# Kernel tuning notes

Hardware: AMD Instinct MI355X
Metric: run time of the kernel (lower is better)

The kernel has to match this reference:

```python
import jax, jax.numpy as jnp
import numpy as np

SEQ_LEN = 256
DT = 0.05
PI4 = float(np.pi / 4)
B = 16384


def _policy(h, W1, b1, W2, b2, W3, b3, W4, b4):
    h = jax.nn.relu(h @ W1 + b1)
    h = jax.nn.relu(h @ W2 + b2)
    h = jax.nn.relu(h @ W3 + b3)
    return jnp.tanh(h @ W4 + b4)


def setup_inputs() -> dict:
    key = jax.random.key(0)
    ks = jax.random.split(key, 11)
    return {
        "state": jax.random.normal(ks[0], (B, 6), jnp.float32),
        "pstate": jax.random.normal(ks[1], (B, 6), jnp.float32),
        "target": jax.random.normal(ks[2], (B, 6), jnp.float32),
        "W1": jax.random.normal(ks[3], (12, 50), jnp.float32) * 0.2,
        "b1": jax.random.normal(ks[4], (50,), jnp.float32) * 0.1,
        "W2": jax.random.normal(ks[5], (50, 50), jnp.float32) * 0.14,
        "b2": jax.random.normal(ks[6], (50,), jnp.float32) * 0.1,
        "W3": jax.random.normal(ks[7], (50, 50), jnp.float32) * 0.14,
        "b3": jax.random.normal(ks[8], (50,), jnp.float32) * 0.1,
        "W4": jax.random.normal(ks[9], (50, 2), jnp.float32) * 0.14,
        "b4": jax.random.normal(ks[10], (2,), jnp.float32) * 0.1,
    }


def reference(state, pstate, target, W1, b1, W2, b2, W3, b3, W4, b4):
    # target duplicated to match concat(pstate, state): [B, 12]
    tgt = jnp.concatenate([target, target], axis=-1)

    def step(carry, _):
        pstate, state = carry
        u = _policy(jnp.concatenate([pstate, state], axis=-1) - tgt,
                    W1, b1, W2, b2, W3, b3, W4, b4) * 0.5  # [B, 2]
        x, y, c, s, v, w = (state[:, i] for i in range(6))
        cw = jnp.cos(w * DT)
        sw = jnp.sin(w * DT)
        x = x + v * c * DT
        y = y + v * s * DT
        c_new = c * cw - s * sw
        # NOTE: original torch code uses the *updated* c when updating s
        s_new = s * cw + c_new * sw
        v = jnp.clip(v + u[:, 0] * DT, -0.1, 0.3)
        w = jnp.clip(w + u[:, 1] * DT, -PI4, PI4)
        new_state = jnp.stack([x, y, c_new, s_new, v, w], axis=-1)
        return (state, new_state), (u, new_state)

    _, (u_seq, states) = jax.lax.scan(step, (pstate, state), None, length=SEQ_LEN)
    # u_seq: [SEQ_LEN, B, 2], states: [SEQ_LEN, B, 6]
    return u_seq, states
```

## Files before the change

### kernel.cpp

```cpp
#include <hip/hip_runtime.h>
#include <hip/hip_bf16.h>
#include <stdint.h>
#include <math.h>

#define SEQ_LEN 256
#define BATCH   16384

typedef _Float16 half8  __attribute__((ext_vector_type(8)));
typedef _Float16 half2t __attribute__((ext_vector_type(2)));
typedef __attribute__((ext_vector_type(4))) float    floatx4;
typedef __attribute__((ext_vector_type(4))) uint32_t uint4v;
typedef __attribute__((ext_vector_type(2))) float    float2v;

__device__ __forceinline__ uint32_t pkh(float a, float b){
    return __builtin_bit_cast(uint32_t, __builtin_amdgcn_cvt_pkrtz(a, b));
}
__device__ __forceinline__ float h16lo(uint32_t p){
    return (float)__builtin_bit_cast(half2t, p)[0];
}
__device__ __forceinline__ float h16hi(uint32_t p){
    return (float)__builtin_bit_cast(half2t, p)[1];
}
__device__ __forceinline__ half8 ashfrag(uint4v u){ return __builtin_bit_cast(half8, u); }
#define MFMA_H(A,B,C) __builtin_amdgcn_mfma_f32_16x16x32_f16((A),(B),(C),0,0,0)

__global__ __launch_bounds__(64, 1) void mbrl_mfma(
    const float* __restrict__ state0, const float* __restrict__ pstate0,
    const float* __restrict__ target,
    const float* __restrict__ W1, const float* __restrict__ b1,
    const float* __restrict__ W2, const float* __restrict__ b2,
    const float* __restrict__ W3, const float* __restrict__ b3,
    const float* __restrict__ W4, const float* __restrict__ b4,
    float* __restrict__ out)
{
    const int lane = threadIdx.x & 63;
    const int c16  = lane & 15;
    const int phi  = lane >> 4;
    const int rowg = (int)blockIdx.x * 16 + c16;

    half8 P1[4], Q1[4];
#pragma unroll
    for (int t = 0; t < 4; ++t){
        const int j = 16*t + c16;
        uint4v uP, uQ;
#pragma unroll
        for (int v = 0; v < 4; ++v){
            float pP[2], pQ[2];
#pragma unroll
            for (int q = 0; q < 2; ++q){
                const int kk = 16*(v>>1) + 4*phi + 2*(v&1) + q;
                float w = 0.f;
                if (j < 50){
                    if (kk < 12)                  w = W1[kk*50 + j];
                    else if (kk == 12)            w = b1[j];
                    else if (kk >= 16 && kk < 28) w = W1[(kk-16)*50 + j];
                }
                float s0 = (float)(_Float16)w;
                pP[q] = s0; pQ[q] = w - s0;
            }
            uP[v] = pkh(pP[0], pP[1]);
            uQ[v] = pkh(pQ[0], pQ[1]);
        }
        P1[t] = ashfrag(uP); Q1[t] = ashfrag(uQ);
    }

    half8 A2[2][4][2], A3[2][4][2];
#pragma unroll
    for (int t = 0; t < 4; ++t){
        const int j = 16*t + c16;
#pragma unroll
        for (int kt = 0; kt < 2; ++kt){
            uint4v u2[2], u3[2];
#pragma unroll
            for (int v = 0; v < 4; ++v){
                float p2[2][2], p3[2][2];
#pragma unroll
                for (int q = 0; q < 2; ++q){
                    const int kk = 32*kt + 16*(v>>1) + 4*phi + 2*(v&1) + q;
                    float w2v = 0.f, w3v = 0.f;
                    if (j < 50){
                        if (kk < 50){ w2v = W2[kk*50 + j]; w3v = W3[kk*50 + j]; }
                        else if (kk == 50){ w2v = b2[j]; w3v = b3[j]; }
                    }
                    float a0 = (float)(_Float16)w2v;
                    float c0s = (float)(_Float16)w3v;
                    p2[0][q] = a0;  p2[1][q] = w2v - a0;
                    p3[0][q] = c0s; p3[1][q] = w3v - c0s;
                }
#pragma unroll
                for (int s = 0; s < 2; ++s){
                    u2[s][v] = pkh(p2[s][0], p2[s][1]);
                    u3[s][v] = pkh(p3[s][0], p3[s][1]);
                }
            }
#pragma unroll
            for (int s = 0; s < 2; ++s){
                A2[s][t][kt] = ashfrag(u2[s]); A3[s][t][kt] = ashfrag(u3[s]);
            }
        }
    }

    float w4a[16], w4b[16];
#pragma unroll
    for (int t = 0; t < 4; ++t)
#pragma unroll
        for (int r = 0; r < 4; ++r){
            const int j = 16*t + 4*phi + r;
            w4a[4*t+r] = (j < 50) ? W4[j*2 + 0] : 0.f;
            w4b[4*t+r] = (j < 50) ? W4[j*2 + 1] : 0.f;
        }
    const float b40 = b4[0], b41 = b4[1];

    float ps[6], ss[6], tg[6];
#pragma unroll
    for (int i = 0; i < 6; ++i){
        ps[i] = pstate0[(size_t)rowg*6 + i];
        ss[i] = state0 [(size_t)rowg*6 + i];
        tg[i] = target [(size_t)rowg*6 + i];
    }

    const float DT  = 0.05f;
    const float PI4 = 0.78539816339744830962f;
    const floatx4 z4 = {0.f,0.f,0.f,0.f};
    const uint32_t ONE_H = 0x00003C00u;

    float* uout = out + (size_t)rowg * 2;
    float* sout = out + (size_t)SEQ_LEN * BATCH * 2 + (size_t)rowg * 6;

    half8 H0a,H0b,H1a,H1b;

#define SPLITH(HA,HB,PK0,PK1) do{                                      \
        PK0 = pkh((HA),(HB));                                          \
        float _a = h16lo(PK0), _b = h16hi(PK0);                        \
        PK1 = pkh((HA)-_a, (HB)-_b);                                   \
    }while(0)

#define MKH(cc0,cc1,cc2,cc3) do{                                                             \
        uint4v u0a,u0b,u1a,u1b;                                                              \
        { float ha=fmaxf(cc0[0],0.f), hb=fmaxf(cc0[1],0.f); SPLITH(ha,hb,u0a[0],u1a[0]); }   \
        { float ha=fmaxf(cc0[2],0.f), hb=fmaxf(cc0[3],0.f); SPLITH(ha,hb,u0a[1],u1a[1]); }   \
        { float ha=fmaxf(cc1[0],0.f), hb=fmaxf(cc1[1],0.f); SPLITH(ha,hb,u0a[2],u1a[2]); }   \
        { float ha=fmaxf(cc1[2],0.f), hb=fmaxf(cc1[3],0.f); SPLITH(ha,hb,u0a[3],u1a[3]); }   \
        { float ha=fmaxf(cc2[0],0.f), hb=fmaxf(cc2[1],0.f); SPLITH(ha,hb,u0b[0],u1b[0]); }   \
        { float ha=fmaxf(cc2[2],0.f), hb=fmaxf(cc2[3],0.f); SPLITH(ha,hb,u0b[1],u1b[1]); }   \
        { float ha=fmaxf(cc3[0],0.f), hb=fmaxf(cc3[1],0.f); SPLITH(ha,hb,u0b[2],u1b[2]); }   \
        { float ha=fmaxf(cc3[2],0.f), hb=fmaxf(cc3[3],0.f); SPLITH(ha,hb,u0b[3],u1b[3]); }   \
        if (phi == 0){ u0b[3]=ONE_H; u1b[3]=0u; }                  \
        H0a=ashfrag(u0a); H0b=ashfrag(u0b); H1a=ashfrag(u1a); H1b=ashfrag(u1b);              \
    }while(0)

#define HID_RR(A)                                                                            \
        c0=MFMA_H(A[0][0][0],H0a,z4); c1=MFMA_H(A[0][1][0],H0a,z4); c2=MFMA_H(A[0][2][0],H0a,z4); c3=MFMA_H(A[0][3][0],H0a,z4); \
        c0=MFMA_H(A[0][0][1],H0b,c0); c1=MFMA_H(A[0][1][1],H0b,c1); c2=MFMA_H(A[0][2][1],H0b,c2); c3=MFMA_H(A[0][3][1],H0b,c3); \
        c0=MFMA_H(A[0][0][0],H1a,c0); c1=MFMA_H(A[0][1][0],H1a,c1); c2=MFMA_H(A[0][2][0],H1a,c2); c3=MFMA_H(A[0][3][0],H1a,c3); \
        c0=MFMA_H(A[0][0][1],H1b,c0); c1=MFMA_H(A[0][1][1],H1b,c1); c2=MFMA_H(A[0][2][1],H1b,c2); c3=MFMA_H(A[0][3][1],H1b,c3); \
        c0=MFMA_H(A[1][0][0],H0a,c0); c1=MFMA_H(A[1][1][0],H0a,c1); c2=MFMA_H(A[1][2][0],H0a,c2); c3=MFMA_H(A[1][3][0],H0a,c3); \
        c0=MFMA_H(A[1][0][1],H0b,c0); c1=MFMA_H(A[1][1][1],H0b,c1); c2=MFMA_H(A[1][2][1],H0b,c2); c3=MFMA_H(A[1][3][1],H0b,c3);

#define L4ACC(CT,T) do{                                                   \
        _Pragma("unroll")                                                 \
        for (int r = 0; r < 4; ++r){                                      \
            float hv = fmaxf(CT[r], 0.f);                                 \
            z0p = fmaf(hv, w4a[4*(T)+r], z0p);                            \
            z1p = fmaf(hv, w4b[4*(T)+r], z1p);                            \
        }                                                                 \
    }while(0)

    for (int t = 0; t < SEQ_LEN; ++t){
        float X0=ps[0]-tg[0], X1=ps[1]-tg[1], X2=ps[2]-tg[2];
        float X3=ps[3]-tg[3], X4=ps[4]-tg[4], X5=ps[5]-tg[5];
        float X6=ss[0]-tg[0], X7=ss[1]-tg[1], X8=ss[2]-tg[2];
        float X9=ss[3]-tg[3], X10=ss[4]-tg[4], X11=ss[5]-tg[5];
        float xs0 = (phi==0)?X0:(phi==1)?X4:(phi==2)?X8 :0.f;
        float xs1 = (phi==0)?X1:(phi==1)?X5:(phi==2)?X9 :0.f;
        float xs2 = (phi==0)?X2:(phi==1)?X6:(phi==2)?X10:0.f;
        float xs3 = (phi==0)?X3:(phi==1)?X7:(phi==2)?X11:0.f;
        uint32_t pH01,pL01,pH23,pL23;
        SPLITH(xs0,xs1,pH01,pL01);
        SPLITH(xs2,xs3,pH23,pL23);
        uint4v f1;
        f1[0] = (phi==3) ? ONE_H : pH01;
        f1[1] = (phi==3) ? 0u    : pH23;
        f1[2] = (phi==3) ? 0u    : pL01;
        f1[3] = (phi==3) ? 0u    : pL23;
        const half8 F1 = ashfrag(f1);

        floatx4 c0, c1, c2, c3;
        c0=MFMA_H(P1[0],F1,z4); c1=MFMA_H(P1[1],F1,z4); c2=MFMA_H(P1[2],F1,z4); c3=MFMA_H(P1[3],F1,z4);
        c0=MFMA_H(Q1[0],F1,c0); c1=MFMA_H(Q1[1],F1,c1); c2=MFMA_H(Q1[2],F1,c2); c3=MFMA_H(Q1[3],F1,c3);
        MKH(c0,c1,c2,c3);

        HID_RR(A2)
        MKH(c0,c1,c2,c3);

        HID_RR(A3)

        float z0p = 0.f, z1p = 0.f;
        L4ACC(c0,0); L4ACC(c1,1); L4ACC(c2,2); L4ACC(c3,3);
        z0p += __shfl_xor(z0p, 16, 64);
        z1p += __shfl_xor(z1p, 16, 64);
        z0p += __shfl_xor(z0p, 32, 64);
        z1p += __shfl_xor(z1p, 32, 64);
        float zz0 = z0p + b40;
        float zz1 = z1p + b41;

        float u0 = 0.5f - __builtin_amdgcn_rcpf(__expf(2.0f*zz0) + 1.0f);
        float u1 = 0.5f - __builtin_amdgcn_rcpf(__expf(2.0f*zz1) + 1.0f);

        float th = ss[5]*DT, t2 = th*th;
        float sw = th * fmaf(t2, fmaf(t2, 8.3333333333e-3f, -1.6666666667e-1f), 1.0f);
        float cw = fmaf(t2, fmaf(t2, fmaf(t2, -1.3888888889e-3f, 4.1666666667e-2f), -0.5f), 1.0f);
        float nx = fmaf(ss[4]*ss[2], DT, ss[0]);
        float ny = fmaf(ss[4]*ss[3], DT, ss[1]);
        float nc = ss[2]*cw - ss[3]*sw;
        float ns = fmaf(ss[3], cw, nc*sw);
        float nv = fminf(fmaxf(fmaf(u0, DT, ss[4]), -0.1f), 0.3f);
        float nw = fminf(fmaxf(fmaf(u1, DT, ss[5]), -PI4), PI4);

        if (phi == 0){
            float2v uv  = {u0, u1};
            *(float2v*)uout = uv;
            float2v s01 = {nx, ny}, s23 = {nc, ns}, s45 = {nv, nw};
            *(float2v*)(sout    ) = s01;
            *(float2v*)(sout + 2) = s23;
            *(float2v*)(sout + 4) = s45;
        }
        uout += (size_t)BATCH * 2;
        sout += (size_t)BATCH * 6;

#pragma unroll
        for (int i = 0; i < 6; ++i) ps[i] = ss[i];
        ss[0]=nx; ss[1]=ny; ss[2]=nc; ss[3]=ns; ss[4]=nv; ss[5]=nw;
    }
#undef MKH
#undef SPLITH
#undef HID_RR
#undef L4ACC
}

extern "C" void kernel_launch(void* const* d_in, const int* in_sizes, int n_in,
                              void* d_out, int out_size, void* d_ws, size_t ws_size,
                              hipStream_t stream)
{
    const float* state  = (const float*)d_in[0];
    const float* pstate = (const float*)d_in[1];
    const float* target = (const float*)d_in[2];
    const float* W1 = (const float*)d_in[3];
    const float* b1 = (const float*)d_in[4];
    const float* W2 = (const float*)d_in[5];
    const float* b2 = (const float*)d_in[6];
    const float* W3 = (const float*)d_in[7];
    const float* b3 = (const float*)d_in[8];
    const float* W4 = (const float*)d_in[9];
    const float* b4 = (const float*)d_in[10];
    float* out = (float*)d_out;

    dim3 grid(BATCH/16), block(64);
    mbrl_mfma<<<grid, block, 0, stream>>>(state, pstate, target,
                                          W1,b1,W2,b2,W3,b3,W4,b4, out);
}
```

Before: 287.5 us.

## Split hidden-unit tiles across two wavefronts with LDS exchange per layer

Each block now runs two wavefronts on the same 16 batch rows, and each wave computes half of the 64 hidden-unit tiles. The halves of each activation vector and of the final layer's partial sums are exchanged through shared memory, with a block barrier at every layer. The goal is to shorten the serial MFMA dependency chain per timestep and halve per-wave weight registers, allowing higher occupancy. In exchange it adds three __syncthreads and LDS round trips per step over 256 sequential steps, and it doubles the wave count.

```diff
diff --git a/kernel.cpp b/kernel.cpp
--- a/kernel.cpp
+++ b/kernel.cpp
@@ -24,7 +24,7 @@
 __device__ __forceinline__ half8 ashfrag(uint4v u){ return __builtin_bit_cast(half8, u); }
 #define MFMA_H(A,B,C) __builtin_amdgcn_mfma_f32_16x16x32_f16((A),(B),(C),0,0,0)
 
-__global__ __launch_bounds__(64, 1) void mbrl_mfma(
+__global__ __launch_bounds__(128, 2) void mbrl_mfma2(
     const float* __restrict__ state0, const float* __restrict__ pstate0,
     const float* __restrict__ target,
     const float* __restrict__ W1, const float* __restrict__ b1,
@@ -33,15 +33,21 @@
     const float* __restrict__ W4, const float* __restrict__ b4,
     float* __restrict__ out)
 {
-    const int lane = threadIdx.x & 63;
+    const int tid  = threadIdx.x;
+    const int wid  = tid >> 6;
+    const int lane = tid & 63;
     const int c16  = lane & 15;
     const int phi  = lane >> 4;
     const int rowg = (int)blockIdx.x * 16 + c16;
 
-    half8 P1[4], Q1[4];
-#pragma unroll
-    for (int t = 0; t < 4; ++t){
-        const int j = 16*t + c16;
+    __shared__ __align__(16) uint4v  xA[2][2][64];
+    __shared__ __align__(16) uint4v  xB[2][2][64];
+    __shared__ __align__(16) float2v zxch[2][64];
+
+    half8 P1[2], Q1[2];
+#pragma unroll
+    for (int tl = 0; tl < 2; ++tl){
+        const int j = 16*(2*wid + tl) + c16;
         uint4v uP, uQ;
 #pragma unroll
         for (int v = 0; v < 4; ++v){
@@ -61,13 +67,13 @@
             uP[v] = pkh(pP[0], pP[1]);
             uQ[v] = pkh(pQ[0], pQ[1]);
         }
-        P1[t] = ashfrag(uP); Q1[t] = ashfrag(uQ);
-    }
-
-    half8 A2[2][4][2], A3[2][4][2];
-#pragma unroll
-    for (int t = 0; t < 4; ++t){
-        const int j = 16*t + c16;
+        P1[tl] = ashfrag(uP); Q1[tl] = ashfrag(uQ);
+    }
+
+    half8 A2[2][2][2], A3[2][2][2];
+#pragma unroll
+    for (int tl = 0; tl < 2; ++tl){
+        const int j = 16*(2*wid + tl) + c16;
 #pragma unroll
         for (int kt = 0; kt < 2; ++kt){
             uint4v u2[2], u3[2];
@@ -82,7 +88,7 @@
                         if (kk < 50){ w2v = W2[kk*50 + j]; w3v = W3[kk*50 + j]; }
                         else if (kk == 50){ w2v = b2[j]; w3v = b3[j]; }
                     }
-                    float a0 = (float)(_Float16)w2v;
+                    float a0  = (float)(_Float16)w2v;
                     float c0s = (float)(_Float16)w3v;
                     p2[0][q] = a0;  p2[1][q] = w2v - a0;
                     p3[0][q] = c0s; p3[1][q] = w3v - c0s;
@@ -95,19 +101,19 @@
             }
 #pragma unroll
             for (int s = 0; s < 2; ++s){
-                A2[s][t][kt] = ashfrag(u2[s]); A3[s][t][kt] = ashfrag(u3[s]);
+                A2[s][tl][kt] = ashfrag(u2[s]); A3[s][tl][kt] = ashfrag(u3[s]);
             }
         }
     }
 
-    float w4a[16], w4b[16];
-#pragma unroll
-    for (int t = 0; t < 4; ++t)
+    float w4a[8], w4b[8];
+#pragma unroll
+    for (int tl = 0; tl < 2; ++tl)
 #pragma unroll
         for (int r = 0; r < 4; ++r){
-            const int j = 16*t + 4*phi + r;
-            w4a[4*t+r] = (j < 50) ? W4[j*2 + 0] : 0.f;
-            w4b[4*t+r] = (j < 50) ? W4[j*2 + 1] : 0.f;
+            const int j = 32*wid + 16*tl + 4*phi + r;
+            w4a[4*tl+r] = (j < 50) ? W4[j*2 + 0] : 0.f;
+            w4b[4*tl+r] = (j < 50) ? W4[j*2 + 1] : 0.f;
         }
     const float b40 = b4[0], b41 = b4[1];
 
@@ -126,8 +132,6 @@
 
     float* uout = out + (size_t)rowg * 2;
     float* sout = out + (size_t)SEQ_LEN * BATCH * 2 + (size_t)rowg * 6;
-
-    half8 H0a,H0b,H1a,H1b;
 
 #define SPLITH(HA,HB,PK0,PK1) do{                                      \
         PK0 = pkh((HA),(HB));                                          \
@@ -135,36 +139,31 @@
         PK1 = pkh((HA)-_a, (HB)-_b);                                   \
     }while(0)
 
-#define MKH(cc0,cc1,cc2,cc3) do{                                                             \
-        uint4v u0a,u0b,u1a,u1b;                                                              \
-        { float ha=fmaxf(cc0[0],0.f), hb=fmaxf(cc0[1],0.f); SPLITH(ha,hb,u0a[0],u1a[0]); }   \
-        { float ha=fmaxf(cc0[2],0.f), hb=fmaxf(cc0[3],0.f); SPLITH(ha,hb,u0a[1],u1a[1]); }   \
-        { float ha=fmaxf(cc1[0],0.f), hb=fmaxf(cc1[1],0.f); SPLITH(ha,hb,u0a[2],u1a[2]); }   \
-        { float ha=fmaxf(cc1[2],0.f), hb=fmaxf(cc1[3],0.f); SPLITH(ha,hb,u0a[3],u1a[3]); }   \
-        { float ha=fmaxf(cc2[0],0.f), hb=fmaxf(cc2[1],0.f); SPLITH(ha,hb,u0b[0],u1b[0]); }   \
-        { float ha=fmaxf(cc2[2],0.f), hb=fmaxf(cc2[3],0.f); SPLITH(ha,hb,u0b[1],u1b[1]); }   \
-        { float ha=fmaxf(cc3[0],0.f), hb=fmaxf(cc3[1],0.f); SPLITH(ha,hb,u0b[2],u1b[2]); }   \
-        { float ha=fmaxf(cc3[2],0.f), hb=fmaxf(cc3[3],0.f); SPLITH(ha,hb,u0b[3],u1b[3]); }   \
-        if (phi == 0){ u0b[3]=ONE_H; u1b[3]=0u; }                  \
-        H0a=ashfrag(u0a); H0b=ashfrag(u0b); H1a=ashfrag(u1a); H1b=ashfrag(u1b);              \
+#define PACKH(CA,CB,U0,U1) do{                                                           \
+        { float ha=fmaxf(CA[0],0.f), hb=fmaxf(CA[1],0.f); SPLITH(ha,hb,U0[0],U1[0]); }   \
+        { float ha=fmaxf(CA[2],0.f), hb=fmaxf(CA[3],0.f); SPLITH(ha,hb,U0[1],U1[1]); }   \
+        { float ha=fmaxf(CB[0],0.f), hb=fmaxf(CB[1],0.f); SPLITH(ha,hb,U0[2],U1[2]); }   \
+        { float ha=fmaxf(CB[2],0.f), hb=fmaxf(CB[3],0.f); SPLITH(ha,hb,U0[3],U1[3]); }   \
+        if (wid == 1 && phi == 0){ U0[3] = ONE_H; U1[3] = 0u; }     \
     }while(0)
 
-#define HID_RR(A)                                                                            \
-        c0=MFMA_H(A[0][0][0],H0a,z4); c1=MFMA_H(A[0][1][0],H0a,z4); c2=MFMA_H(A[0][2][0],H0a,z4); c3=MFMA_H(A[0][3][0],H0a,z4); \
-        c0=MFMA_H(A[0][0][1],H0b,c0); c1=MFMA_H(A[0][1][1],H0b,c1); c2=MFMA_H(A[0][2][1],H0b,c2); c3=MFMA_H(A[0][3][1],H0b,c3); \
-        c0=MFMA_H(A[0][0][0],H1a,c0); c1=MFMA_H(A[0][1][0],H1a,c1); c2=MFMA_H(A[0][2][0],H1a,c2); c3=MFMA_H(A[0][3][0],H1a,c3); \
-        c0=MFMA_H(A[0][0][1],H1b,c0); c1=MFMA_H(A[0][1][1],H1b,c1); c2=MFMA_H(A[0][2][1],H1b,c2); c3=MFMA_H(A[0][3][1],H1b,c3); \
-        c0=MFMA_H(A[1][0][0],H0a,c0); c1=MFMA_H(A[1][1][0],H0a,c1); c2=MFMA_H(A[1][2][0],H0a,c2); c3=MFMA_H(A[1][3][0],H0a,c3); \
-        c0=MFMA_H(A[1][0][1],H0b,c0); c1=MFMA_H(A[1][1][1],H0b,c1); c2=MFMA_H(A[1][2][1],H0b,c2); c3=MFMA_H(A[1][3][1],H0b,c3);
-
-#define L4ACC(CT,T) do{                                                   \
-        _Pragma("unroll")                                                 \
-        for (int r = 0; r < 4; ++r){                                      \
-            float hv = fmaxf(CT[r], 0.f);                                 \
-            z0p = fmaf(hv, w4a[4*(T)+r], z0p);                            \
-            z1p = fmaf(hv, w4b[4*(T)+r], z1p);                            \
-        }                                                                 \
+#define XCHG(R)  do{                                                    \
+        R[wid][0][lane] = u0; R[wid][1][lane] = u1;                     \
+        __syncthreads();                                                \
+        uint4v o0 = R[wid^1][0][lane], o1 = R[wid^1][1][lane];          \
+        if (wid == 0){ H0a=ashfrag(u0); H1a=ashfrag(u1);                \
+                       H0b=ashfrag(o0); H1b=ashfrag(o1); }              \
+        else         { H0a=ashfrag(o0); H1a=ashfrag(o1);                \
+                       H0b=ashfrag(u0); H1b=ashfrag(u1); }              \
     }while(0)
+
+#define HID(A)                                                              \
+        ca=MFMA_H(A[0][0][0],H0a,z4); cb=MFMA_H(A[0][1][0],H0a,z4);         \
+        ca=MFMA_H(A[0][0][1],H0b,ca); cb=MFMA_H(A[0][1][1],H0b,cb);         \
+        ca=MFMA_H(A[0][0][0],H1a,ca); cb=MFMA_H(A[0][1][0],H1a,cb);         \
+        ca=MFMA_H(A[0][0][1],H1b,ca); cb=MFMA_H(A[0][1][1],H1b,cb);         \
+        ca=MFMA_H(A[1][0][0],H0a,ca); cb=MFMA_H(A[1][1][0],H0a,cb);         \
+        ca=MFMA_H(A[1][0][1],H0b,ca); cb=MFMA_H(A[1][1][1],H0b,cb);
 
     for (int t = 0; t < SEQ_LEN; ++t){
         float X0=ps[0]-tg[0], X1=ps[1]-tg[1], X2=ps[2]-tg[2];
@@ -180,23 +179,44 @@
         SPLITH(xs2,xs3,pH23,pL23);
         uint4v f1;
         f1[0] = (phi==3) ? ONE_H : pH01;
-        f1[1] = (phi==3) ? 0u    : pH23;
-        f1[2] = (phi==3) ? 0u    : pL01;
-        f1[3] = (phi==3) ? 0u    : pL23;
+        f1[1] = pH23;
+        f1[2] = pL01;
+        f1[3] = pL23;
         const half8 F1 = ashfrag(f1);
 
-        floatx4 c0, c1, c2, c3;
-        c0=MFMA_H(P1[0],F1,z4); c1=MFMA_H(P1[1],F1,z4); c2=MFMA_H(P1[2],F1,z4); c3=MFMA_H(P1[3],F1,z4);
-        c0=MFMA_H(Q1[0],F1,c0); c1=MFMA_H(Q1[1],F1,c1); c2=MFMA_H(Q1[2],F1,c2); c3=MFMA_H(Q1[3],F1,c3);
-        MKH(c0,c1,c2,c3);
-
-        HID_RR(A2)
-        MKH(c0,c1,c2,c3);
-
-        HID_RR(A3)
+        floatx4 ca, cb;
+        ca=MFMA_H(P1[0],F1,z4); cb=MFMA_H(P1[1],F1,z4);
+        ca=MFMA_H(Q1[0],F1,ca); cb=MFMA_H(Q1[1],F1,cb);
+
+        half8 H0a,H0b,H1a,H1b;
+        uint4v u0, u1;
+        PACKH(ca,cb,u0,u1);
+        XCHG(xA);
+
+        HID(A2)
+        PACKH(ca,cb,u0,u1);
+        XCHG(xB);
+
+        HID(A3)
 
         float z0p = 0.f, z1p = 0.f;
-        L4ACC(c0,0); L4ACC(c1,1); L4ACC(c2,2); L4ACC(c3,3);
+#pragma unroll
+        for (int r = 0; r < 4; ++r){
+            float hv = fmaxf(ca[r], 0.f);
+            z0p = fmaf(hv, w4a[r],   z0p);
+            z1p = fmaf(hv, w4b[r],   z1p);
+        }
+#pragma unroll
+        for (int r = 0; r < 4; ++r){
+            float hv = fmaxf(cb[r], 0.f);
+            z0p = fmaf(hv, w4a[4+r], z0p);
+            z1p = fmaf(hv, w4b[4+r], z1p);
+        }
+        float2v zp = {z0p, z1p};
+        zxch[wid][lane] = zp;
+        __syncthreads();
+        float2v oz = zxch[wid^1][lane];
+        z0p += oz[0]; z1p += oz[1];
         z0p += __shfl_xor(z0p, 16, 64);
         z1p += __shfl_xor(z1p, 16, 64);
         z0p += __shfl_xor(z0p, 32, 64);
@@ -204,8 +224,8 @@
         float zz0 = z0p + b40;
         float zz1 = z1p + b41;
 
-        float u0 = 0.5f - __builtin_amdgcn_rcpf(__expf(2.0f*zz0) + 1.0f);
-        float u1 = 0.5f - __builtin_amdgcn_rcpf(__expf(2.0f*zz1) + 1.0f);
+        float u0v = 0.5f - __builtin_amdgcn_rcpf(__expf(2.0f*zz0) + 1.0f);
+        float u1v = 0.5f - __builtin_amdgcn_rcpf(__expf(2.0f*zz1) + 1.0f);
 
         float th = ss[5]*DT, t2 = th*th;
         float sw = th * fmaf(t2, fmaf(t2, 8.3333333333e-3f, -1.6666666667e-1f), 1.0f);
@@ -214,11 +234,11 @@
         float ny = fmaf(ss[4]*ss[3], DT, ss[1]);
         float nc = ss[2]*cw - ss[3]*sw;
         float ns = fmaf(ss[3], cw, nc*sw);
-        float nv = fminf(fmaxf(fmaf(u0, DT, ss[4]), -0.1f), 0.3f);
-        float nw = fminf(fmaxf(fmaf(u1, DT, ss[5]), -PI4), PI4);
-
-        if (phi == 0){
-            float2v uv  = {u0, u1};
+        float nv = fminf(fmaxf(fmaf(u0v, DT, ss[4]), -0.1f), 0.3f);
+        float nw = fminf(fmaxf(fmaf(u1v, DT, ss[5]), -PI4), PI4);
+
+        if (wid == 0 && phi == 0){
+            float2v uv  = {u0v, u1v};
             *(float2v*)uout = uv;
             float2v s01 = {nx, ny}, s23 = {nc, ns}, s45 = {nv, nw};
             *(float2v*)(sout    ) = s01;
@@ -232,10 +252,10 @@
         for (int i = 0; i < 6; ++i) ps[i] = ss[i];
         ss[0]=nx; ss[1]=ny; ss[2]=nc; ss[3]=ns; ss[4]=nv; ss[5]=nw;
     }
-#undef MKH
 #undef SPLITH
-#undef HID_RR
-#undef L4ACC
+#undef PACKH
+#undef XCHG
+#undef HID
 }
 
 extern "C" void kernel_launch(void* const* d_in, const int* in_sizes, int n_in,
@@ -255,7 +275,7 @@
     const float* b4 = (const float*)d_in[10];
     float* out = (float*)d_out;
 
-    dim3 grid(BATCH/16), block(64);
-    mbrl_mfma<<<grid, block, 0, stream>>>(state, pstate, target,
-                                          W1,b1,W2,b2,W3,b3,W4,b4, out);
-}
+    dim3 grid(BATCH/16), block(128);
+    mbrl_mfma2<<<grid, block, 0, stream>>>(state, pstate, target,
+                                           W1,b1,W2,b2,W3,b3,W4,b4, out);
+}
```

Result: slower. 351.6 us (+22.3%).
